# Performance work log

Measured on AMD Instinct MI355X. Metric: run time of the kernel, lower is better.

## Reference

```python
import jax, jax.numpy as jnp
import numpy as np

N = 50000      # total nodes
E = 800000     # total edges
B = 512        # number of graphs (batch size)
D_IN, H, D_OUT = 5, 96, 192
EPS = 1e-5


def setup_inputs() -> dict:
    key = jax.random.key(0)
    ks = jax.random.split(key, 20)
    s = lambda d: 1.0 / np.sqrt(d)
    inp = {
        "x": jax.random.normal(ks[0], (N, D_IN), jnp.float32),
        "edge_index": jax.random.randint(ks[1], (2, E), 0, N, jnp.int64),
        "batch": jnp.sort(jax.random.randint(ks[2], (N,), 0, B, jnp.int64)),
        "W_in": jax.random.normal(ks[3], (D_IN, H), jnp.float32) * s(D_IN),
        "b_in": jnp.zeros((H,), jnp.float32),
        "W1": jax.random.normal(ks[4], (H, H), jnp.float32) * s(H),
        "b1": jnp.zeros((H,), jnp.float32),
        "g1": jnp.ones((H,), jnp.float32),
        "be1": jnp.zeros((H,), jnp.float32),
        "W2": jax.random.normal(ks[5], (H, H), jnp.float32) * s(H),
        "b2": jnp.zeros((H,), jnp.float32),
        "g2": jnp.ones((H,), jnp.float32),
        "be2": jnp.zeros((H,), jnp.float32),
        "W_out": jax.random.normal(ks[6], (H, D_OUT), jnp.float32) * s(H),
        "b_out": jnp.zeros((D_OUT,), jnp.float32),
        "ln_g": jnp.ones((D_OUT,), jnp.float32),
        "ln_b": jnp.zeros((D_OUT,), jnp.float32),
    }
    return inp


def gcn_conv(h, W, b, src, dst):
    # PyG GCNConv: h' = D^{-1/2} (A + I) D^{-1/2} (h W) + b, deg from self-looped graph
    h = h @ W                                           # [N, H]
    deg = jnp.ones((N,), h.dtype).at[dst].add(jnp.ones((E,), h.dtype))
    dinv = jax.lax.rsqrt(deg)                           # [N]
    coef = dinv[src] * dinv[dst]                        # [E]
    agg = jnp.zeros_like(h).at[dst].add(h[src] * coef[:, None])
    agg = agg + h * (dinv * dinv)[:, None]              # self-loop term
    return agg + b


def batch_norm(x, g, b):
    m = x.mean(0)
    v = x.var(0)
    return g * (x - m) * jax.lax.rsqrt(v + EPS) + b


def reference(x, edge_index, batch, W_in, b_in, W1, b1, g1, be1, W2, b2, g2, be2,
              W_out, b_out, ln_g, ln_b):
    src, dst = edge_index[0], edge_index[1]
    h = jax.nn.relu(x @ W_in + b_in)
    for (W, bb, g, be) in ((W1, b1, g1, be1), (W2, b2, g2, be2)):
        r = h
        h = gcn_conv(h, W, bb, src, dst)
        h = jax.nn.relu(batch_norm(h, g, be))           # dropout = identity (eval)
        h = h + r
    counts = jnp.zeros((B,), h.dtype).at[batch].add(1.0)
    pooled = jax.ops.segment_sum(h, batch, num_segments=B)
    pooled = pooled / jnp.maximum(counts, 1.0)[:, None]  # global_mean_pool [B, H]
    out = pooled @ W_out + b_out                         # [B, D_OUT]
    mu = out.mean(-1, keepdims=True)
    var = out.var(-1, keepdims=True)
    return ln_g * (out - mu) * jax.lax.rsqrt(var + EPS) + ln_b
```

## Files before the change

### kernel.cpp

```cpp
#include <hip/hip_runtime.h>
#include <hip/hip_bf16.h>
#include <stdint.h>

#define NN 50000
#define EE 800000
#define BB 512
#define HH 96
#define DIN 5
#define DOUT 192
#define EPSV 1e-5f
#define NBANK 32
#define HWS 64
#define NB_GATHER 3125
#define NBLK_SCAN ((NN + 1023) / 1024)
#define NBUK 512
#define BUKN 98
#define FILLB 128
#define FCHUNK (EE / FILLB)

__device__ inline float blo(uint32_t w) { return __uint_as_float(w << 16); }
__device__ inline float bhi(uint32_t w) { return __uint_as_float(w & 0xffff0000u); }
__device__ inline uint32_t packbf(float a, float b) {
    uint32_t ua = __float_as_uint(a); ua += 0x7fffu + ((ua >> 16) & 1u);
    uint32_t ub = __float_as_uint(b); ub += 0x7fffu + ((ub >> 16) & 1u);
    return (ua >> 16) | (ub & 0xffff0000u);
}

__global__ __launch_bounds__(256) void k_bhist(const int* __restrict__ dst,
                                               int* __restrict__ bkcnt) {
    __shared__ int hist[NBUK];
    int tid = threadIdx.x;
    for (int j = tid; j < NBUK; j += 256) hist[j] = 0;
    __syncthreads();
    int e0 = blockIdx.x * FCHUNK;
    for (int e = e0 + tid; e < e0 + FCHUNK; e += 256) atomicAdd(&hist[dst[e] / BUKN], 1);
    __syncthreads();
    for (int j = tid; j < NBUK; j += 256) if (hist[j]) atomicAdd(&bkcnt[j], hist[j]);
}

__global__ __launch_bounds__(256) void k_bscan(const int* __restrict__ bkcnt,
                                               int* __restrict__ bkbase,
                                               int* __restrict__ bkcur,
                                               float* __restrict__ stats,
                                               int* __restrict__ row_ptr) {
    __shared__ int sc[NBUK + 1];
    int t = threadIdx.x;
    for (int i = t; i < 2 * NBANK * 192; i += 256) stats[i] = 0.0f;
    for (int j = t; j < NBUK; j += 256) sc[j] = bkcnt[j];
    __syncthreads();
    if (t == 0) {
        int c = 0;
        for (int j = 0; j < NBUK; ++j) { int s = sc[j]; sc[j] = c; c += s; }
        sc[NBUK] = c;
        row_ptr[NN] = c;
    }
    __syncthreads();
    for (int j = t; j <= NBUK; j += 256) bkbase[j] = sc[j];
    for (int j = t; j < NBUK; j += 256) bkcur[j] = sc[j];
}

__global__ __launch_bounds__(256) void k_bscat(const int* __restrict__ src,
                                               const int* __restrict__ dst,
                                               int* __restrict__ bkcur,
                                               uint32_t* __restrict__ ebuf) {
    __shared__ int hist[NBUK], bbase[NBUK], cnt[NBUK];
    int tid = threadIdx.x;
    int e0 = blockIdx.x * FCHUNK, e1 = e0 + FCHUNK;
    for (int j = tid; j < NBUK; j += 256) { hist[j] = 0; cnt[j] = 0; }
    __syncthreads();
    for (int e = e0 + tid; e < e1; e += 256) atomicAdd(&hist[dst[e] / BUKN], 1);
    __syncthreads();
    for (int j = tid; j < NBUK; j += 256) bbase[j] = hist[j] ? atomicAdd(&bkcur[j], hist[j]) : 0;
    __syncthreads();
    for (int e = e0 + tid; e < e1; e += 256) {
        int d = dst[e];
        int b = d / BUKN;
        int off = atomicAdd(&cnt[b], 1);
        ebuf[bbase[b] + off] = (uint32_t)src[e] | ((uint32_t)(d - b * BUKN) << 16);
    }
}

__global__ __launch_bounds__(256) void k_csr(const uint32_t* __restrict__ ebuf,
                                             const int* __restrict__ bkbase,
                                             int* __restrict__ row_ptr,
                                             int* __restrict__ col,
                                             int* __restrict__ degi,
                                             float* __restrict__ dinv) {
    __shared__ int cnt[BUKN], base[BUKN], lcur[BUKN];
    int b = blockIdx.x, tid = threadIdx.x;
    int node0 = b * BUKN;
    if (node0 >= NN) return;
    int nn = min(BUKN, NN - node0);
    int ebase = bkbase[b], eend = bkbase[b + 1];
    for (int j = tid; j < nn; j += 256) { cnt[j] = 0; lcur[j] = 0; }
    __syncthreads();
    for (int i = ebase + tid; i < eend; i += 256) atomicAdd(&cnt[ebuf[i] >> 16], 1);
    __syncthreads();
    if (tid == 0) {
        int c = 0;
        for (int j = 0; j < nn; ++j) { base[j] = c; c += cnt[j]; }
    }
    __syncthreads();
    for (int j = tid; j < nn; j += 256) {
        row_ptr[node0 + j] = ebase + base[j];
        degi[node0 + j] = cnt[j];
        dinv[node0 + j] = rsqrtf((float)cnt[j] + 1.0f);
    }
    for (int i = ebase + tid; i < eend; i += 256) {
        uint32_t w = ebuf[i];
        int dr = (int)(w >> 16);
        int off = atomicAdd(&lcur[dr], 1);
        col[ebase + base[dr] + off] = (int)(w & 0xffffu);
    }
}

__global__ __launch_bounds__(1024) void k_dhist(const int* __restrict__ degi,
                                                int* __restrict__ histg) {
    __shared__ int dh[64];
    int tid = threadIdx.x;
    if (tid < 64) dh[tid] = 0;
    __syncthreads();
    int i = blockIdx.x * 1024 + tid;
    if (i < NN) atomicAdd(&dh[min(degi[i], 63)], 1);
    __syncthreads();
    if (tid < 64) histg[blockIdx.x * 64 + tid] = dh[tid];
}

__global__ __launch_bounds__(64) void k_dscan(int* __restrict__ histg) {
    __shared__ int tot[64], binbase[64];
    int t = threadIdx.x;
    int s = 0;
    for (int k = 0; k < NBLK_SCAN; ++k) s += histg[k * 64 + t];
    tot[t] = s;
    __syncthreads();
    if (t == 0) {
        int c = 0;
        for (int b2 = 0; b2 < 64; ++b2) { binbase[b2] = c; c += tot[b2]; }
    }
    __syncthreads();
    int c = binbase[t];
    for (int k = 0; k < NBLK_SCAN; ++k) {
        int tmp = histg[k * 64 + t];
        histg[k * 64 + t] = c;
        c += tmp;
    }
}

__global__ __launch_bounds__(1024) void k_dperm(const int* __restrict__ degi,
                                                const int* __restrict__ histg,
                                                int* __restrict__ perm) {
    __shared__ int lcur[64];
    int tid = threadIdx.x;
    if (tid < 64) lcur[tid] = histg[blockIdx.x * 64 + tid];
    __syncthreads();
    int i = blockIdx.x * 1024 + tid;
    if (i < NN) {
        int pos = atomicAdd(&lcur[min(degi[i], 63)], 1);
        perm[pos] = i;
    }
}

__device__ inline void store48(uint32_t* __restrict__ hwb, int gr, int q,
                               const float* acc, float dval) {
    uint32_t wv[12];
#pragma unroll
    for (int p = 0; p < 12; ++p) wv[p] = packbf(acc[2 * p] * dval, acc[2 * p + 1] * dval);
    uint4* dstp = reinterpret_cast<uint4*>(&hwb[(size_t)gr * HWS + q * 12]);
    dstp[0] = make_uint4(wv[0], wv[1], wv[2], wv[3]);
    dstp[1] = make_uint4(wv[4], wv[5], wv[6], wv[7]);
    dstp[2] = make_uint4(wv[8], wv[9], wv[10], wv[11]);
}

__global__ __launch_bounds__(256) void k_gemm_in(const float* __restrict__ x,
                                                 const float* __restrict__ Win,
                                                 const float* __restrict__ bin,
                                                 const float* __restrict__ W1,
                                                 const float* __restrict__ dinv,
                                                 float* __restrict__ h0,
                                                 uint32_t* __restrict__ hwb) {
    __shared__ float sA[64][100];
    __shared__ float sW[96 * 96];
    __shared__ float sWin[5 * 96];
    __shared__ float sbin[96];
    int tid = threadIdx.x;
    int row0 = blockIdx.x * 64;

    for (int i = tid; i < 96 * 96; i += 256) sW[i] = W1[i];
    for (int i = tid; i < 5 * 96; i += 256) sWin[i] = Win[i];
    if (tid < 96) sbin[tid] = bin[tid];
    __syncthreads();

    int r = tid >> 2, q = tid & 3;
    int j0 = q * 24;
    int gr = row0 + r;

    {
        float xv[5];
#pragma unroll
        for (int k = 0; k < DIN; ++k) xv[k] = (gr < NN) ? x[gr * DIN + k] : 0.0f;
        float hv[24];
#pragma unroll
        for (int jj = 0; jj < 24; ++jj) {
            float acc = sbin[j0 + jj];
#pragma unroll
            for (int k = 0; k < DIN; ++k) acc += xv[k] * sWin[k * 96 + j0 + jj];
            hv[jj] = fmaxf(acc, 0.0f);
            sA[r][j0 + jj] = hv[jj];
        }
        if (gr < NN) {
#pragma unroll
            for (int jj = 0; jj < 24; jj += 4)
                *reinterpret_cast<float4*>(&h0[(size_t)gr * 96 + j0 + jj]) =
                    make_float4(hv[jj], hv[jj + 1], hv[jj + 2], hv[jj + 3]);
        }
    }
    __syncthreads();

    float acc[24];
#pragma unroll
    for (int jj = 0; jj < 24; ++jj) acc[jj] = 0.0f;
    for (int k = 0; k < 96; ++k) {
        float a = sA[r][k];
#pragma unroll
        for (int jj = 0; jj < 24; ++jj) acc[jj] += a * sW[k * 96 + j0 + jj];
    }
    if (gr < NN) store48(hwb, gr, q, acc, dinv[gr]);
}

__global__ __launch_bounds__(256) void k_gather(const uint32_t* __restrict__ hwb,
                                                const float* __restrict__ dinv,
                                                const int* __restrict__ row_ptr,
                                                const int* __restrict__ col,
                                                const int* __restrict__ perm,
                                                float* __restrict__ agg,
                                                float* __restrict__ stats) {
    int tid = threadIdx.x;
    int t = tid & 15, slot = tid >> 4;
    int n = perm[blockIdx.x * 16 + slot];

    const uint32_t* rn = hwb + (size_t)n * HWS;
    uint2 w01 = *reinterpret_cast<const uint2*>(rn + 2 * t);
    uint32_t w2 = rn[32 + t];
    float a0 = blo(w01.x), a1 = bhi(w01.x);
    float a2 = blo(w01.y), a3 = bhi(w01.y);
    float a4 = blo(w2),    a5 = bhi(w2);

    int beg = row_ptr[n], end = row_ptr[n + 1];
    int p = beg;
    for (; p + 3 < end; p += 4) {
        int s0 = col[p], s1 = col[p + 1], s2 = col[p + 2], s3 = col[p + 3];
        const uint32_t* r0 = hwb + (size_t)s0 * HWS;
        const uint32_t* r1 = hwb + (size_t)s1 * HWS;
        const uint32_t* r2 = hwb + (size_t)s2 * HWS;
        const uint32_t* r3 = hwb + (size_t)s3 * HWS;
        uint2 u0 = *reinterpret_cast<const uint2*>(r0 + 2 * t); uint32_t v0 = r0[32 + t];
        uint2 u1 = *reinterpret_cast<const uint2*>(r1 + 2 * t); uint32_t v1 = r1[32 + t];
        uint2 u2 = *reinterpret_cast<const uint2*>(r2 + 2 * t); uint32_t v2 = r2[32 + t];
        uint2 u3 = *reinterpret_cast<const uint2*>(r3 + 2 * t); uint32_t v3 = r3[32 + t];
        a0 += blo(u0.x); a1 += bhi(u0.x); a2 += blo(u0.y); a3 += bhi(u0.y);
        a4 += blo(v0);   a5 += bhi(v0);
        a0 += blo(u1.x); a1 += bhi(u1.x); a2 += blo(u1.y); a3 += bhi(u1.y);
        a4 += blo(v1);   a5 += bhi(v1);
        a0 += blo(u2.x); a1 += bhi(u2.x); a2 += blo(u2.y); a3 += bhi(u2.y);
        a4 += blo(v2);   a5 += bhi(v2);
        a0 += blo(u3.x); a1 += bhi(u3.x); a2 += blo(u3.y); a3 += bhi(u3.y);
        a4 += blo(v3);   a5 += bhi(v3);
    }
    for (; p < end; ++p) {
        const uint32_t* rs = hwb + (size_t)col[p] * HWS;
        uint2 u = *reinterpret_cast<const uint2*>(rs + 2 * t);
        uint32_t v = rs[32 + t];
        a0 += blo(u.x); a1 += bhi(u.x);
        a2 += blo(u.y); a3 += bhi(u.y);
        a4 += blo(v);   a5 += bhi(v);
    }
    float dn = dinv[n];
    a0 *= dn; a1 *= dn; a2 *= dn; a3 *= dn; a4 *= dn; a5 *= dn;

    float* an = agg + (size_t)n * 96;
    *reinterpret_cast<float4*>(&an[4 * t])      = make_float4(a0, a1, a2, a3);
    *reinterpret_cast<float2*>(&an[64 + 2 * t]) = make_float2(a4, a5);

    __shared__ float red[2][96];
    if (tid < 96) { red[0][tid] = 0.0f; red[1][tid] = 0.0f; }
    __syncthreads();
    int colsv[6] = {4 * t, 4 * t + 1, 4 * t + 2, 4 * t + 3, 64 + 2 * t, 64 + 2 * t + 1};
    float cs[6] = {a0, a1, a2, a3, a4, a5};
#pragma unroll
    for (int k = 0; k < 6; ++k) {
        atomicAdd(&red[0][colsv[k]], cs[k]);
        atomicAdd(&red[1][colsv[k]], cs[k] * cs[k]);
    }
    __syncthreads();
    float* bank = stats + (blockIdx.x & (NBANK - 1)) * 192;
    if (tid < 96) {
        atomicAdd(&bank[tid], red[0][tid]);
        atomicAdd(&bank[96 + tid], red[1][tid]);
    }
}

__global__ __launch_bounds__(256) void k_gemm_bn(const float* __restrict__ agg,
                                                 const float* __restrict__ hprev,
                                                 const float* __restrict__ stats,
                                                 const float* __restrict__ g,
                                                 const float* __restrict__ be,
                                                 const float* __restrict__ W,
                                                 const float* __restrict__ dinv,
                                                 float* __restrict__ hnew,
                                                 uint32_t* __restrict__ hwb) {
    __shared__ float sA[64][100];
    __shared__ float sW[96 * 96];
    __shared__ float ssc[96], ssh[96];
    int tid = threadIdx.x;
    int row0 = blockIdx.x * 64;

    for (int i = tid; i < 96 * 96; i += 256) sW[i] = W[i];
    if (tid < 96) {
        float s = 0.0f, s2 = 0.0f;
#pragma unroll
        for (int k = 0; k < NBANK; ++k) { s += stats[k * 192 + tid]; s2 += stats[k * 192 + 96 + tid]; }
        float m = s * (1.0f / NN);
        float var = s2 * (1.0f / NN) - m * m;
        float sc = g[tid] * rsqrtf(var + EPSV);
        ssc[tid] = sc;
        ssh[tid] = be[tid] - m * sc;
    }
    __syncthreads();

    for (int i = tid; i < 64 * 24; i += 256) {
        int r = i / 24, qq = i % 24;
        int gr = row0 + r, c = qq * 4;
        float4 v = make_float4(0.0f, 0.0f, 0.0f, 0.0f);
        if (gr < NN) {
            float4 a = *reinterpret_cast<const float4*>(&agg[(size_t)gr * 96 + c]);
            float4 pv = *reinterpret_cast<const float4*>(&hprev[(size_t)gr * 96 + c]);
            v.x = fmaxf(a.x * ssc[c]     + ssh[c],     0.0f) + pv.x;
            v.y = fmaxf(a.y * ssc[c + 1] + ssh[c + 1], 0.0f) + pv.y;
            v.z = fmaxf(a.z * ssc[c + 2] + ssh[c + 2], 0.0f) + pv.z;
            v.w = fmaxf(a.w * ssc[c + 3] + ssh[c + 3], 0.0f) + pv.w;
            *reinterpret_cast<float4*>(&hnew[(size_t)gr * 96 + c]) = v;
        }
        *reinterpret_cast<float4*>(&sA[r][c]) = v;
    }
    __syncthreads();

    int r = tid >> 2, q = tid & 3;
    int j0 = q * 24;
    int gr = row0 + r;
    float acc[24];
#pragma unroll
    for (int jj = 0; jj < 24; ++jj) acc[jj] = 0.0f;
    for (int k = 0; k < 96; ++k) {
        float a = sA[r][k];
#pragma unroll
        for (int jj = 0; jj < 24; ++jj) acc[jj] += a * sW[k * 96 + j0 + jj];
    }
    if (gr < NN) store48(hwb, gr, q, acc, dinv[gr]);
}

__device__ inline int lower_bound_i(const int* __restrict__ a, int n, int v) {
    int lo = 0, hi = n;
    while (lo < hi) { int mid = (lo + hi) >> 1; if (a[mid] < v) lo = mid + 1; else hi = mid; }
    return lo;
}

__global__ __launch_bounds__(384) void k_out(const float* __restrict__ agg,
                                             const float* __restrict__ hprev,
                                             const float* __restrict__ stats,
                                             const float* __restrict__ g,
                                             const float* __restrict__ be,
                                             const int* __restrict__ batch,
                                             const float* __restrict__ Wout,
                                             const float* __restrict__ bout,
                                             const float* __restrict__ lg,
                                             const float* __restrict__ lb,
                                             float* __restrict__ out) {
    __shared__ float ssc[96], ssh[96];
    __shared__ float sp4[4][96];
    __shared__ float sp[96];
    __shared__ float svals[192];
    __shared__ float smv[2];
    int b = blockIdx.x, t = threadIdx.x;
    if (t < 96) {
        float s = 0.0f, s2 = 0.0f;
#pragma unroll
        for (int k = 0; k < NBANK; ++k) { s += stats[k * 192 + t]; s2 += stats[k * 192 + 96 + t]; }
        float m = s * (1.0f / NN);
        float var = s2 * (1.0f / NN) - m * m;
        float sc = g[t] * rsqrtf(var + EPSV);
        ssc[t] = sc;
        ssh[t] = be[t] - m * sc;
    }
    int lo = lower_bound_i(batch, NN, b);
    int hi = lower_bound_i(batch, NN, b + 1);
    __syncthreads();

    int colc = t % 96, qr = t / 96;
    float scc = ssc[colc], shc = ssh[colc];
    float accp = 0.0f;
    for (int r = lo + qr; r < hi; r += 4) {
        size_t idx = (size_t)r * 96 + colc;
        accp += fmaxf(agg[idx] * scc + shc, 0.0f) + hprev[idx];
    }
    sp4[qr][colc] = accp;
    __syncthreads();
    if (t < 96) {
        float inv = (hi > lo) ? 1.0f / (float)(hi - lo) : 0.0f;
        sp[t] = (sp4[0][t] + sp4[1][t] + sp4[2][t] + sp4[3][t]) * inv;
    }
    __syncthreads();

    float acc = 0.0f;
    if (t < 192) {
        acc = bout[t];
        for (int k = 0; k < 96; ++k) acc += sp[k] * Wout[k * 192 + t];
        svals[t] = acc;
    }
    __syncthreads();
    if (t < 64) {
        float a0 = svals[t], a1 = svals[t + 64], a2 = svals[t + 128];
        float s = a0 + a1 + a2;
        float s2 = a0 * a0 + a1 * a1 + a2 * a2;
        for (int o = 32; o > 0; o >>= 1) {
            s += __shfl_down(s, o, 64);
            s2 += __shfl_down(s2, o, 64);
        }
        if (t == 0) { smv[0] = s * (1.0f / 192.0f); smv[1] = s2 * (1.0f / 192.0f); }
    }
    __syncthreads();
    if (t < 192) {
        float m = smv[0];
        float var = smv[1] - m * m;
        float rr = rsqrtf(var + EPSV);
        out[b * 192 + t] = lg[t] * (acc - m) * rr + lb[t];
    }
}

extern "C" void kernel_launch(void* const* d_in, const int* in_sizes, int n_in,
                              void* d_out, int out_size, void* d_ws, size_t ws_size,
                              hipStream_t stream) {
    const float* x    = (const float*)d_in[0];
    const int*   ei   = (const int*)  d_in[1];
    const int*   batch= (const int*)  d_in[2];
    const float* Win  = (const float*)d_in[3];
    const float* bin  = (const float*)d_in[4];
    const float* W1   = (const float*)d_in[5];
    const float* g1   = (const float*)d_in[7];
    const float* be1  = (const float*)d_in[8];
    const float* W2   = (const float*)d_in[9];
    const float* g2   = (const float*)d_in[11];
    const float* be2  = (const float*)d_in[12];
    const float* Wout = (const float*)d_in[13];
    const float* bout = (const float*)d_in[14];
    const float* lg   = (const float*)d_in[15];
    const float* lb   = (const float*)d_in[16];
    const int* src = ei;
    const int* dst = ei + EE;

    float*    ws_f   = (float*)d_ws;
    float*    h0     = ws_f;
    float*    h1     = h0 + (size_t)NN * HH;
    float*    agg    = h1 + (size_t)NN * HH;
    float*    dinv   = agg + (size_t)NN * HH;
    float*    stats  = dinv + NN;
    uint32_t* hwb    = (uint32_t*)(stats + 2 * NBANK * 192);
    int*      degi   = (int*)(hwb + (size_t)NN * HWS);
    int*      histg  = degi + NN;
    int*      row_ptr= histg + NBLK_SCAN * 64;
    int*      perm   = row_ptr + NN + 1;
    int*      bkcnt  = perm + NN;
    int*      bkbase = bkcnt + NBUK;
    int*      bkcur  = bkbase + NBUK + 1;
    int*      col    = bkcur + NBUK;
    uint32_t* ebuf   = (uint32_t*)agg;

    const int TB = 256;
    float* stats1 = stats;
    float* stats2 = stats + NBANK * 192;

    hipMemsetAsync(bkcnt, 0, NBUK * sizeof(int), stream);
    k_bhist<<<FILLB, TB, 0, stream>>>(dst, bkcnt);
    k_bscan<<<1, TB, 0, stream>>>(bkcnt, bkbase, bkcur, stats, row_ptr);
    k_bscat<<<FILLB, TB, 0, stream>>>(src, dst, bkcur, ebuf);
    k_csr<<<NBUK, TB, 0, stream>>>(ebuf, bkbase, row_ptr, col, degi, dinv);
    k_dhist<<<NBLK_SCAN, 1024, 0, stream>>>(degi, histg);
    k_dscan<<<1, 64, 0, stream>>>(histg);
    k_dperm<<<NBLK_SCAN, 1024, 0, stream>>>(degi, histg, perm);

    k_gemm_in<<<(NN + 63) / 64, TB, 0, stream>>>(x, Win, bin, W1, dinv, h0, hwb);
    k_gather<<<NB_GATHER, TB, 0, stream>>>(hwb, dinv, row_ptr, col, perm, agg, stats1);

    k_gemm_bn<<<(NN + 63) / 64, TB, 0, stream>>>(agg, h0, stats1, g1, be1, W2, dinv, h1, hwb);
    k_gather<<<NB_GATHER, TB, 0, stream>>>(hwb, dinv, row_ptr, col, perm, agg, stats2);

    k_out<<<BB, 384, 0, stream>>>(agg, h1, stats2, g2, be2, batch, Wout, bout, lg, lb,
                                  (float*)d_out);
}
```

Measured before the change: 281.5 us.

## Drop degree-sorted node permutation and register-tile the dense GEMMs

Removes the degree histogram, scan and permutation kernels, so the gather kernels now process nodes in natural order instead of degree-sorted order. This saves three kernel launches and their passes over the nodes, at the cost of possible load imbalance between wavefront slots that get nodes of very different degree. Separately, both 96x96 GEMM kernels switch from one row by 24 columns per thread to a 4x6 register tile over a transposed activation tile in shared memory. This increases reuse of each shared-memory load but makes the bf16 output stores narrower (3 words per row instead of 16-byte vectors).

```diff
diff --git a/kernel.cpp b/kernel.cpp
--- a/kernel.cpp
+++ b/kernel.cpp
@@ -12,7 +12,6 @@
 #define NBANK 32
 #define HWS 64
 #define NB_GATHER 3125
-#define NBLK_SCAN ((NN + 1023) / 1024)
 #define NBUK 512
 #define BUKN 98
 #define FILLB 128
@@ -84,7 +83,6 @@
                                              const int* __restrict__ bkbase,
                                              int* __restrict__ row_ptr,
                                              int* __restrict__ col,
-                                             int* __restrict__ degi,
                                              float* __restrict__ dinv) {
     __shared__ int cnt[BUKN], base[BUKN], lcur[BUKN];
     int b = blockIdx.x, tid = threadIdx.x;
@@ -103,7 +101,6 @@
     __syncthreads();
     for (int j = tid; j < nn; j += 256) {
         row_ptr[node0 + j] = ebase + base[j];
-        degi[node0 + j] = cnt[j];
         dinv[node0 + j] = rsqrtf((float)cnt[j] + 1.0f);
     }
     for (int i = ebase + tid; i < eend; i += 256) {
@@ -112,63 +109,6 @@
         int off = atomicAdd(&lcur[dr], 1);
         col[ebase + base[dr] + off] = (int)(w & 0xffffu);
     }
-}
-
-__global__ __launch_bounds__(1024) void k_dhist(const int* __restrict__ degi,
-                                                int* __restrict__ histg) {
-    __shared__ int dh[64];
-    int tid = threadIdx.x;
-    if (tid < 64) dh[tid] = 0;
-    __syncthreads();
-    int i = blockIdx.x * 1024 + tid;
-    if (i < NN) atomicAdd(&dh[min(degi[i], 63)], 1);
-    __syncthreads();
-    if (tid < 64) histg[blockIdx.x * 64 + tid] = dh[tid];
-}
-
-__global__ __launch_bounds__(64) void k_dscan(int* __restrict__ histg) {
-    __shared__ int tot[64], binbase[64];
-    int t = threadIdx.x;
-    int s = 0;
-    for (int k = 0; k < NBLK_SCAN; ++k) s += histg[k * 64 + t];
-    tot[t] = s;
-    __syncthreads();
-    if (t == 0) {
-        int c = 0;
-        for (int b2 = 0; b2 < 64; ++b2) { binbase[b2] = c; c += tot[b2]; }
-    }
-    __syncthreads();
-    int c = binbase[t];
-    for (int k = 0; k < NBLK_SCAN; ++k) {
-        int tmp = histg[k * 64 + t];
-        histg[k * 64 + t] = c;
-        c += tmp;
-    }
-}
-
-__global__ __launch_bounds__(1024) void k_dperm(const int* __restrict__ degi,
-                                                const int* __restrict__ histg,
-                                                int* __restrict__ perm) {
-    __shared__ int lcur[64];
-    int tid = threadIdx.x;
-    if (tid < 64) lcur[tid] = histg[blockIdx.x * 64 + tid];
-    __syncthreads();
-    int i = blockIdx.x * 1024 + tid;
-    if (i < NN) {
-        int pos = atomicAdd(&lcur[min(degi[i], 63)], 1);
-        perm[pos] = i;
-    }
-}
-
-__device__ inline void store48(uint32_t* __restrict__ hwb, int gr, int q,
-                               const float* acc, float dval) {
-    uint32_t wv[12];
-#pragma unroll
-    for (int p = 0; p < 12; ++p) wv[p] = packbf(acc[2 * p] * dval, acc[2 * p + 1] * dval);
-    uint4* dstp = reinterpret_cast<uint4*>(&hwb[(size_t)gr * HWS + q * 12]);
-    dstp[0] = make_uint4(wv[0], wv[1], wv[2], wv[3]);
-    dstp[1] = make_uint4(wv[4], wv[5], wv[6], wv[7]);
-    dstp[2] = make_uint4(wv[8], wv[9], wv[10], wv[11]);
 }
 
 __global__ __launch_bounds__(256) void k_gemm_in(const float* __restrict__ x,
@@ -178,65 +118,79 @@
                                                  const float* __restrict__ dinv,
                                                  float* __restrict__ h0,
                                                  uint32_t* __restrict__ hwb) {
-    __shared__ float sA[64][100];
+    __shared__ float sAT[96][68];
     __shared__ float sW[96 * 96];
-    __shared__ float sWin[5 * 96];
-    __shared__ float sbin[96];
     int tid = threadIdx.x;
     int row0 = blockIdx.x * 64;
 
     for (int i = tid; i < 96 * 96; i += 256) sW[i] = W1[i];
-    for (int i = tid; i < 5 * 96; i += 256) sWin[i] = Win[i];
-    if (tid < 96) sbin[tid] = bin[tid];
-    __syncthreads();
-
-    int r = tid >> 2, q = tid & 3;
-    int j0 = q * 24;
-    int gr = row0 + r;
 
     {
+        int r = tid >> 2, q = tid & 3;
+        int j0q = q * 24;
+        int gr = row0 + r;
         float xv[5];
 #pragma unroll
         for (int k = 0; k < DIN; ++k) xv[k] = (gr < NN) ? x[gr * DIN + k] : 0.0f;
         float hv[24];
 #pragma unroll
         for (int jj = 0; jj < 24; ++jj) {
-            float acc = sbin[j0 + jj];
-#pragma unroll
-            for (int k = 0; k < DIN; ++k) acc += xv[k] * sWin[k * 96 + j0 + jj];
+            float acc = bin[j0q + jj];
+#pragma unroll
+            for (int k = 0; k < DIN; ++k) acc += xv[k] * Win[k * 96 + j0q + jj];
             hv[jj] = fmaxf(acc, 0.0f);
-            sA[r][j0 + jj] = hv[jj];
+            sAT[j0q + jj][r] = hv[jj];
         }
         if (gr < NN) {
 #pragma unroll
             for (int jj = 0; jj < 24; jj += 4)
-                *reinterpret_cast<float4*>(&h0[(size_t)gr * 96 + j0 + jj]) =
+                *reinterpret_cast<float4*>(&h0[(size_t)gr * 96 + j0q + jj]) =
                     make_float4(hv[jj], hv[jj + 1], hv[jj + 2], hv[jj + 3]);
         }
     }
     __syncthreads();
 
-    float acc[24];
-#pragma unroll
-    for (int jj = 0; jj < 24; ++jj) acc[jj] = 0.0f;
+    int tc = tid & 15, tr = tid >> 4;
+    int r0 = tr * 4, j0 = tc * 6;
+    float acc[4][6];
+#pragma unroll
+    for (int i = 0; i < 4; ++i)
+#pragma unroll
+        for (int j = 0; j < 6; ++j) acc[i][j] = 0.0f;
+
     for (int k = 0; k < 96; ++k) {
-        float a = sA[r][k];
-#pragma unroll
-        for (int jj = 0; jj < 24; ++jj) acc[jj] += a * sW[k * 96 + j0 + jj];
-    }
-    if (gr < NN) store48(hwb, gr, q, acc, dinv[gr]);
+        float4 a = *reinterpret_cast<const float4*>(&sAT[k][r0]);
+        const float* wr = &sW[k * 96 + j0];
+        float b0 = wr[0], b1 = wr[1], b2 = wr[2], b3 = wr[3], b4 = wr[4], b5 = wr[5];
+        float av[4] = {a.x, a.y, a.z, a.w};
+#pragma unroll
+        for (int i = 0; i < 4; ++i) {
+            acc[i][0] += av[i] * b0; acc[i][1] += av[i] * b1; acc[i][2] += av[i] * b2;
+            acc[i][3] += av[i] * b3; acc[i][4] += av[i] * b4; acc[i][5] += av[i] * b5;
+        }
+    }
+#pragma unroll
+    for (int i = 0; i < 4; ++i) {
+        int gr = row0 + r0 + i;
+        if (gr < NN) {
+            float dv = dinv[gr];
+            uint32_t* wp = &hwb[(size_t)gr * HWS + tc * 3];
+            wp[0] = packbf(acc[i][0] * dv, acc[i][1] * dv);
+            wp[1] = packbf(acc[i][2] * dv, acc[i][3] * dv);
+            wp[2] = packbf(acc[i][4] * dv, acc[i][5] * dv);
+        }
+    }
 }
 
 __global__ __launch_bounds__(256) void k_gather(const uint32_t* __restrict__ hwb,
                                                 const float* __restrict__ dinv,
                                                 const int* __restrict__ row_ptr,
                                                 const int* __restrict__ col,
-                                                const int* __restrict__ perm,
                                                 float* __restrict__ agg,
                                                 float* __restrict__ stats) {
     int tid = threadIdx.x;
     int t = tid & 15, slot = tid >> 4;
-    int n = perm[blockIdx.x * 16 + slot];
+    int n = blockIdx.x * 16 + slot;
 
     const uint32_t* rn = hwb + (size_t)n * HWS;
     uint2 w01 = *reinterpret_cast<const uint2*>(rn + 2 * t);
@@ -308,7 +262,7 @@
                                                  const float* __restrict__ dinv,
                                                  float* __restrict__ hnew,
                                                  uint32_t* __restrict__ hwb) {
-    __shared__ float sA[64][100];
+    __shared__ float sAT[96][68];
     __shared__ float sW[96 * 96];
     __shared__ float ssc[96], ssh[96];
     int tid = threadIdx.x;
@@ -340,22 +294,40 @@
             v.w = fmaxf(a.w * ssc[c + 3] + ssh[c + 3], 0.0f) + pv.w;
             *reinterpret_cast<float4*>(&hnew[(size_t)gr * 96 + c]) = v;
         }
-        *reinterpret_cast<float4*>(&sA[r][c]) = v;
-    }
-    __syncthreads();
-
-    int r = tid >> 2, q = tid & 3;
-    int j0 = q * 24;
-    int gr = row0 + r;
-    float acc[24];
-#pragma unroll
-    for (int jj = 0; jj < 24; ++jj) acc[jj] = 0.0f;
+        sAT[c][r] = v.x; sAT[c + 1][r] = v.y; sAT[c + 2][r] = v.z; sAT[c + 3][r] = v.w;
+    }
+    __syncthreads();
+
+    int tc = tid & 15, tr = tid >> 4;
+    int r0 = tr * 4, j0 = tc * 6;
+    float acc[4][6];
+#pragma unroll
+    for (int i = 0; i < 4; ++i)
+#pragma unroll
+        for (int j = 0; j < 6; ++j) acc[i][j] = 0.0f;
+
     for (int k = 0; k < 96; ++k) {
-        float a = sA[r][k];
-#pragma unroll
-        for (int jj = 0; jj < 24; ++jj) acc[jj] += a * sW[k * 96 + j0 + jj];
-    }
-    if (gr < NN) store48(hwb, gr, q, acc, dinv[gr]);
+        float4 a = *reinterpret_cast<const float4*>(&sAT[k][r0]);
+        const float* wr = &sW[k * 96 + j0];
+        float b0 = wr[0], b1 = wr[1], b2 = wr[2], b3 = wr[3], b4 = wr[4], b5 = wr[5];
+        float av[4] = {a.x, a.y, a.z, a.w};
+#pragma unroll
+        for (int i = 0; i < 4; ++i) {
+            acc[i][0] += av[i] * b0; acc[i][1] += av[i] * b1; acc[i][2] += av[i] * b2;
+            acc[i][3] += av[i] * b3; acc[i][4] += av[i] * b4; acc[i][5] += av[i] * b5;
+        }
+    }
+#pragma unroll
+    for (int i = 0; i < 4; ++i) {
+        int gr = row0 + r0 + i;
+        if (gr < NN) {
+            float dv = dinv[gr];
+            uint32_t* wp = &hwb[(size_t)gr * HWS + tc * 3];
+            wp[0] = packbf(acc[i][0] * dv, acc[i][1] * dv);
+            wp[1] = packbf(acc[i][2] * dv, acc[i][3] * dv);
+            wp[2] = packbf(acc[i][4] * dv, acc[i][5] * dv);
+        }
+    }
 }
 
 __device__ inline int lower_bound_i(const int* __restrict__ a, int n, int v) {
@@ -464,11 +436,8 @@
     float*    dinv   = agg + (size_t)NN * HH;
     float*    stats  = dinv + NN;
     uint32_t* hwb    = (uint32_t*)(stats + 2 * NBANK * 192);
-    int*      degi   = (int*)(hwb + (size_t)NN * HWS);
-    int*      histg  = degi + NN;
-    int*      row_ptr= histg + NBLK_SCAN * 64;
-    int*      perm   = row_ptr + NN + 1;
-    int*      bkcnt  = perm + NN;
+    int*      row_ptr= (int*)(hwb + (size_t)NN * HWS);
+    int*      bkcnt  = row_ptr + NN + 1;
     int*      bkbase = bkcnt + NBUK;
     int*      bkcur  = bkbase + NBUK + 1;
     int*      col    = bkcur + NBUK;
@@ -482,16 +451,13 @@
     k_bhist<<<FILLB, TB, 0, stream>>>(dst, bkcnt);
     k_bscan<<<1, TB, 0, stream>>>(bkcnt, bkbase, bkcur, stats, row_ptr);
     k_bscat<<<FILLB, TB, 0, stream>>>(src, dst, bkcur, ebuf);
-    k_csr<<<NBUK, TB, 0, stream>>>(ebuf, bkbase, row_ptr, col, degi, dinv);
-    k_dhist<<<NBLK_SCAN, 1024, 0, stream>>>(degi, histg);
-    k_dscan<<<1, 64, 0, stream>>>(histg);
-    k_dperm<<<NBLK_SCAN, 1024, 0, stream>>>(degi, histg, perm);
+    k_csr<<<NBUK, TB, 0, stream>>>(ebuf, bkbase, row_ptr, col, dinv);
 
     k_gemm_in<<<(NN + 63) / 64, TB, 0, stream>>>(x, Win, bin, W1, dinv, h0, hwb);
-    k_gather<<<NB_GATHER, TB, 0, stream>>>(hwb, dinv, row_ptr, col, perm, agg, stats1);
+    k_gather<<<NB_GATHER, TB, 0, stream>>>(hwb, dinv, row_ptr, col, agg, stats1);
 
     k_gemm_bn<<<(NN + 63) / 64, TB, 0, stream>>>(agg, h0, stats1, g1, be1, W2, dinv, h1, hwb);
-    k_gather<<<NB_GATHER, TB, 0, stream>>>(hwb, dinv, row_ptr, col, perm, agg, stats2);
+    k_gather<<<NB_GATHER, TB, 0, stream>>>(hwb, dinv, row_ptr, col, agg, stats2);
 
     k_out<<<BB, 384, 0, stream>>>(agg, h1, stats2, g2, be2, batch, Wout, bout, lg, lb,
                                   (float*)d_out);
```

Result: faster. 268.7 us (-4.6%).
